# Kernel optimization log

Hardware: AMD Instinct MI355X
Metric: run time of the kernel (lower is better)

Reference implementation:

```python
import jax, jax.numpy as jnp
import numpy as np

B, C, H, W = 2, 256, 64, 64  # C = in_channels; x has 2*C channels
DQ = C // 16


def setup_inputs() -> dict:
    key = jax.random.key(0)
    ks = jax.random.split(key, 10)
    s = 0.05
    return {
        "x": jax.random.normal(ks[0], (B, 2 * C, H, W), dtype=jnp.float32),
        "Wq": jax.random.normal(ks[1], (DQ, C), dtype=jnp.float32) * s,
        "bq": jax.random.normal(ks[2], (DQ,), dtype=jnp.float32) * s,
        "Wk": jax.random.normal(ks[3], (DQ, C), dtype=jnp.float32) * s,
        "bk": jax.random.normal(ks[4], (DQ,), dtype=jnp.float32) * s,
        "Wv": jax.random.normal(ks[5], (C, C), dtype=jnp.float32) * s,
        "bv": jax.random.normal(ks[6], (C,), dtype=jnp.float32) * s,
        "Wpt": jax.random.normal(ks[7], (C, 2 * C), dtype=jnp.float32) * s,
        "bpt": jax.random.normal(ks[8], (C,), dtype=jnp.float32) * s,
        "gamma": jnp.full((1,), 0.5, dtype=jnp.float32),  # original inits to 0; nonzero for a non-trivial output
    }


def _conv1x1(x, Wt, b):
    # 1x1 conv == per-pixel linear map over channels
    return jnp.einsum("bchw,dc->bdhw", x, Wt) + b[None, :, None, None]


def reference(x, Wq, bq, Wk, bk, Wv, bv, Wpt, bpt, gamma):
    n = x.shape[1] // 2
    x1, x2 = x[:, :n], x[:, n:]
    b, c, h, w = x1.shape
    hw = h * w

    def qkv(xi):
        q = _conv1x1(xi, Wq, bq).reshape(b, DQ, hw)   # [B,dq,HW]
        k = _conv1x1(xi, Wk, bk).reshape(b, DQ, hw)   # [B,dq,HW]
        v = _conv1x1(xi, Wv, bv).reshape(b, c, hw)    # [B,C,HW]
        return q, k, v

    q1, k1, v1 = qkv(x1)
    q2, k2, v2 = qkv(x2)

    # attn[b,i,j] = softmax_j( q[:,i] . k[:,j] )  (no scaling, as in original)
    attn1 = jax.nn.softmax(jnp.einsum("bdi,bdj->bij", q1, k1), axis=-1)  # [B,HW,HW]
    attn2 = jax.nn.softmax(jnp.einsum("bdi,bdj->bij", q2, k2), axis=-1)

    def apply_attn(v, attn):
        # out[b,c,i] = sum_j v[b,c,j] * attn[b,i,j]
        return jnp.einsum("bcj,bij->bci", v, attn).reshape(b, c, h, w)

    out11 = apply_attn(v1, attn1)
    out12 = apply_attn(v2, attn1)
    out21 = apply_attn(v1, attn2)
    out22 = apply_attn(v2, attn2)

    o1 = _conv1x1(jnp.concatenate([out11, out12], axis=1), Wpt, bpt)  # [B,C,H,W]
    o2 = _conv1x1(jnp.concatenate([out21, out22], axis=1), Wpt, bpt)

    out = gamma * jnp.concatenate([o1, o2], axis=1) + x
    return out
```

## Files before the change

### kernel.cpp

```cpp
#include <hip/hip_runtime.h>
#include <hip/hip_bf16.h>


#define HW 4096
#define CC 256
#define DQ 16

typedef __hip_bfloat16 bf16;
struct alignas(8) bh4 { bf16 x, y, z, w; };
typedef __bf16 bf16x8 __attribute__((ext_vector_type(8)));
typedef float  f32x4  __attribute__((ext_vector_type(4)));

static __device__ __forceinline__ float b2f(bf16 v) { return __bfloat162float(v); }
static __device__ __forceinline__ float ldf(const void* p, size_t i, bool isb) {
    return isb ? b2f(((const bf16*)p)[i]) : ((const float*)p)[i];
}

static __device__ __forceinline__ void load_lds16(const void* g, void* l) {
    __builtin_amdgcn_global_load_lds(
        (const __attribute__((address_space(1))) unsigned int*)g,
        (__attribute__((address_space(3))) unsigned int*)l, 16, 0, 0);
}

static __device__ __forceinline__ bf16x8 ones8() {
    union { unsigned int u[4]; bf16x8 v; } t;
    t.u[0] = t.u[1] = t.u[2] = t.u[3] = 0x3F803F80u;
    return t.v;
}

__global__ void __launch_bounds__(256)
prep_xt(const void* __restrict__ xsrc,
        const void* __restrict__ Wq_r, const void* __restrict__ bq_r,
        const void* __restrict__ Wk_r, const void* __restrict__ bk_r,
        const void* __restrict__ Wv_r, const void* __restrict__ bv_r,
        const void* __restrict__ Wpt_r, const void* __restrict__ bpt_r,
        const void* __restrict__ gam_r,
        float* __restrict__ bqf, float* __restrict__ bkf, float* __restrict__ gamf,
        bf16* __restrict__ Wqb, bf16* __restrict__ Wkb,
        bf16* __restrict__ McB, float* __restrict__ btot, bf16* __restrict__ Xt,
        const unsigned short* __restrict__ probe) {
    __shared__ float T[64][65];
    int bx = blockIdx.x, tid = threadIdx.x;
    bool isb = probe[0] != 0;
    if (bx < 512) {
        int d = bx >> 1;
        int c = ((bx & 1) << 8) + tid;
        int half = c >> 8, cm = c & 255;
        float acc = 0.f;
        for (int e = 0; e < 256; ++e)
            acc = fmaf(ldf(Wpt_r, (size_t)d * 512 + half * 256 + e, isb),
                       ldf(Wv_r, (size_t)e * 256 + cm, isb), acc);
        McB[d * 512 + c] = __float2bfloat16(acc);
    } else if (bx == 512) {
        int d = tid;
        float acc = ldf(bpt_r, d, isb);
        for (int e = 0; e < 256; ++e)
            acc = fmaf(ldf(Wpt_r, (size_t)d * 512 + e, isb) +
                       ldf(Wpt_r, (size_t)d * 512 + 256 + e, isb),
                       ldf(bv_r, e, isb), acc);
        btot[d] = acc;
    } else if (bx < 545) {
        int id = bx - 513;
        const void* s = id < 16 ? Wq_r : Wk_r;
        bf16* dst = id < 16 ? Wqb : Wkb;
        int i = (id & 15) * 256 + tid;
        dst[i] = __float2bfloat16(ldf(s, i, isb));
    } else if (bx == 545) {
        if (tid < 16) bqf[tid] = ldf(bq_r, tid, isb);
        else if (tid < 32) bkf[tid - 16] = ldf(bk_r, tid - 16, isb);
        else if (tid == 32) gamf[0] = ldf(gam_r, 0, isb);
    } else {
        int id = bx - 546;
        int j0 = (id & 63) * 64, e0 = ((id >> 6) & 7) * 64, b = id >> 9;
        int j_l = tid & 63, er0 = (tid >> 6) * 16;
#pragma unroll
        for (int r = 0; r < 16; ++r) {
            size_t src = ((size_t)(b * 512 + e0 + er0 + r)) * HW + j0 + j_l;
            T[er0 + r][j_l] = ldf(xsrc, src, isb);
        }
        __syncthreads();
        int e_w = tid & 63, jr0 = (tid >> 6) * 16;
#pragma unroll
        for (int r = 0; r < 16; ++r)
            Xt[((size_t)b * HW + j0 + jr0 + r) * 512 + e0 + e_w] =
                __float2bfloat16(T[e_w][jr0 + r]);
    }
}

__global__ void __launch_bounds__(256, 2)
qku(const bf16* __restrict__ Xt,
    const bf16* __restrict__ Wqb, const float* __restrict__ bqf,
    const bf16* __restrict__ Wkb, const float* __restrict__ bkf,
    bf16* __restrict__ Qb, bf16* __restrict__ Kb,
    const bf16* __restrict__ McB, bf16* __restrict__ Ub) {
    __shared__ __align__(16) bf16 sA[64 * 64];
    __shared__ __align__(16) bf16 sB[128 * 64];
    int tid = threadIdx.x;
    int lane = tid & 63, wave = tid >> 6;
    int ln = lane & 15, q = lane >> 4;
    int bx = blockIdx.x;

    if (bx < 256) {
        int bh = bx >> 6;
        int b = bh >> 1, h = bh & 1;
        int j0 = (bx & 63) * 64 + wave * 16;
        bf16x8 aQ[8], aK[8];
#pragma unroll
        for (int kk = 0; kk < 8; ++kk) {
            aQ[kk] = *(const bf16x8*)&Wqb[ln * 256 + kk * 32 + q * 8];
            aK[kk] = *(const bf16x8*)&Wkb[ln * 256 + kk * 32 + q * 8];
        }
        const bf16* Xrow = Xt + ((size_t)b * HW + j0 + ln) * 512 + h * 256;
        f32x4 dQ = {0.f, 0.f, 0.f, 0.f}, dK = {0.f, 0.f, 0.f, 0.f};
#pragma unroll
        for (int kk = 0; kk < 8; ++kk) {
            bf16x8 bxv = *(const bf16x8*)&Xrow[kk * 32 + q * 8];
            dQ = __builtin_amdgcn_mfma_f32_16x16x32_bf16(aQ[kk], bxv, dQ, 0, 0, 0);
            dK = __builtin_amdgcn_mfma_f32_16x16x32_bf16(aK[kk], bxv, dK, 0, 0, 0);
        }
        size_t rowoff = ((size_t)bh * HW + j0 + ln) * 32;
        bh4 oq, ok;
        oq.x = __float2bfloat16(dQ[0] + bqf[q * 4 + 0]);
        oq.y = __float2bfloat16(dQ[1] + bqf[q * 4 + 1]);
        oq.z = __float2bfloat16(dQ[2] + bqf[q * 4 + 2]);
        oq.w = __float2bfloat16(dQ[3] + bqf[q * 4 + 3]);
        ok.x = __float2bfloat16(dK[0] + bkf[q * 4 + 0]);
        ok.y = __float2bfloat16(dK[1] + bkf[q * 4 + 1]);
        ok.z = __float2bfloat16(dK[2] + bkf[q * 4 + 2]);
        ok.w = __float2bfloat16(dK[3] + bkf[q * 4 + 3]);
        bh4 z; z.x = z.y = z.z = z.w = __float2bfloat16(0.f);
        *(bh4*)&Qb[rowoff + q * 4] = oq;
        *(bh4*)&Qb[rowoff + 16 + q * 4] = z;
        *(bh4*)&Kb[rowoff + q * 4] = ok;
        *(bh4*)&Kb[rowoff + 16 + q * 4] = z;
        return;
    }

    int id = bx - 256;
    int wm = (wave >> 1) * 32, wn = (wave & 1) * 64;
    int j0 = (id & 31) * 128, c0 = ((id >> 5) & 3) * 64, b = id >> 7;
    const bf16* Xb = Xt + (size_t)b * HW * 512;
    f32x4 acc[2][4];
#pragma unroll
    for (int mi = 0; mi < 2; ++mi)
#pragma unroll
        for (int ni = 0; ni < 4; ++ni)
#pragma unroll
            for (int r = 0; r < 4; ++r) acc[mi][ni][r] = 0.f;

    for (int e0 = 0; e0 < 512; e0 += 64) {
        __syncthreads();
#pragma unroll
        for (int r = 0; r < 2; ++r) {
            int s = r * 256 + tid;
            int row = s >> 3, jc = s & 7, jg = jc ^ (row & 7);
            load_lds16(McB + (size_t)(c0 + row) * 512 + e0 + jg * 8, sA + s * 8);
        }
#pragma unroll
        for (int r = 0; r < 4; ++r) {
            int s = r * 256 + tid;
            int row = s >> 3, jc = s & 7, jg = jc ^ (row & 7);
            load_lds16(Xb + (size_t)(j0 + row) * 512 + e0 + jg * 8, sB + s * 8);
        }
        __syncthreads();
#pragma unroll
        for (int kh = 0; kh < 2; ++kh) {
            bf16x8 af[2], bfv[4];
#pragma unroll
            for (int mi = 0; mi < 2; ++mi) {
                int row = wm + mi * 16 + ln;
                int jc = (kh * 4 + q) ^ (row & 7);
                af[mi] = *(const bf16x8*)&sA[row * 64 + jc * 8];
            }
#pragma unroll
            for (int ni = 0; ni < 4; ++ni) {
                int row = wn + ni * 16 + ln;
                int jc = (kh * 4 + q) ^ (row & 7);
                bfv[ni] = *(const bf16x8*)&sB[row * 64 + jc * 8];
            }
#pragma unroll
            for (int mi = 0; mi < 2; ++mi)
#pragma unroll
                for (int ni = 0; ni < 4; ++ni)
                    acc[mi][ni] = __builtin_amdgcn_mfma_f32_16x16x32_bf16(
                        af[mi], bfv[ni], acc[mi][ni], 0, 0, 0);
        }
    }
#pragma unroll
    for (int mi = 0; mi < 2; ++mi)
#pragma unroll
        for (int r = 0; r < 4; ++r) {
            int c = c0 + wm + mi * 16 + q * 4 + r;
#pragma unroll
            for (int ni = 0; ni < 4; ++ni) {
                int j = j0 + wn + ni * 16 + ln;
                Ub[((size_t)(b * CC + c)) * HW + j] = __float2bfloat16(acc[mi][ni][r]);
            }
        }
}

__global__ void __launch_bounds__(256, 2)
flash_attn(const bf16* __restrict__ Ub, const bf16* __restrict__ Qb,
           const bf16* __restrict__ Kb, const float* __restrict__ btot,
           const void* __restrict__ xorig, const float* __restrict__ gamf,
           void* __restrict__ outv, const unsigned short* __restrict__ probe) {
    __shared__ __align__(16) bf16 sU[3][128 * 64];
    __shared__ __align__(16) bf16 sK[3][4 * 64 * 8];
    __shared__ __align__(16) bf16 sE[2][64 * 64];
    int tid  = threadIdx.x;
    int lane = tid & 63, wave = tid >> 6;
    int ln = lane & 15, q = lane >> 4;
    int wm = (wave & 1) * 64, wn = (wave >> 1) * 32;
    int i0 = blockIdx.x * 64, c0 = blockIdx.y * 128;
    int bh = blockIdx.z;
    int b = bh >> 1, h = bh & 1;
    const bf16* Ubb = Ub + (size_t)b * CC * HW + (size_t)c0 * HW;
    const bf16* Kbh = Kb + (size_t)bh * HW * 32;
    const bf16x8 ONE = ones8();

    bf16x8 bq = *(const bf16x8*)&Qb[((size_t)bh * HW + i0 + wave * 16 + ln) * 32 + q * 8];

    f32x4 acc[4][2], accS[2];
#pragma unroll
    for (int ni = 0; ni < 2; ++ni) {
#pragma unroll
        for (int r = 0; r < 4; ++r) accS[ni][r] = 0.f;
#pragma unroll
        for (int mi = 0; mi < 4; ++mi)
#pragma unroll
            for (int r = 0; r < 4; ++r) acc[mi][ni][r] = 0.f;
    }

    int i_loc = wave * 16 + ln;
    int wchunk0 = (q >> 1);
    int woff = (q & 1) * 4;

    auto stage_u = [&](int tn, int bufn) {
#pragma unroll
        for (int r = 0; r < 4; ++r) {
            int s = r * 256 + tid;
            int row = s >> 3, jc = s & 7, jg = jc ^ (row & 7);
            load_lds16(Ubb + (size_t)row * HW + tn * 64 + jg * 8, &sU[bufn][s * 8]);
        }
    };
    auto stage_k = [&](int tn, int bufn) {
        load_lds16(Kbh + ((size_t)(tn * 64 + (tid >> 6) * 16 + (tid & 15))) * 32
                       + ((tid >> 4) & 3) * 8,
                   &sK[bufn][tid * 8]);
    };

    stage_u(0, 0);
    stage_k(0, 0);
    stage_k(1, 1);
    asm volatile("s_waitcnt vmcnt(0)" ::: "memory");
    __builtin_amdgcn_sched_barrier(0);
    __builtin_amdgcn_s_barrier();
    __builtin_amdgcn_sched_barrier(0);

    int bu_r = 0, bu_s = 1, bk_r = 0, bk_s = 2;
    for (int t = 0; t < 64; ++t) {
        stage_u((t + 1) & 63, bu_s);
        stage_k((t + 2) & 63, bk_s);

        const bf16* sKc = sK[bk_r];
        bf16* sEc = sE[t & 1];
#pragma unroll
        for (int js = 0; js < 4; ++js) {
            bf16x8 ak = *(const bf16x8*)&sKc[(js * 64 + lane) * 8];
            f32x4 d = {0.f, 0.f, 0.f, 0.f};
            d = __builtin_amdgcn_mfma_f32_16x16x32_bf16(ak, bq, d, 0, 0, 0);
            bh4 o;
            o.x = __float2bfloat16(__expf(d[0]));
            o.y = __float2bfloat16(__expf(d[1]));
            o.z = __float2bfloat16(__expf(d[2]));
            o.w = __float2bfloat16(__expf(d[3]));
            int chunk = (js * 2 + wchunk0) ^ (i_loc & 7);
            *(bh4*)&sEc[i_loc * 64 + chunk * 8 + woff] = o;
        }

        asm volatile("s_waitcnt vmcnt(5) lgkmcnt(0)" ::: "memory");
        __builtin_amdgcn_sched_barrier(0);
        __builtin_amdgcn_s_barrier();
        __builtin_amdgcn_sched_barrier(0);

        const bf16* sUc = sU[bu_r];
        __builtin_amdgcn_s_setprio(1);
#pragma unroll
        for (int kh = 0; kh < 2; ++kh) {
            bf16x8 af[4], bfv[2];
#pragma unroll
            for (int mi = 0; mi < 4; ++mi) {
                int row = wm + mi * 16 + ln;
                int jc = (kh * 4 + q) ^ (row & 7);
                af[mi] = *(const bf16x8*)&sUc[row * 64 + jc * 8];
            }
#pragma unroll
            for (int ni = 0; ni < 2; ++ni) {
                int row = wn + ni * 16 + ln;
                int jc = (kh * 4 + q) ^ (row & 7);
                bfv[ni] = *(const bf16x8*)&sEc[row * 64 + jc * 8];
            }
#pragma unroll
            for (int ni = 0; ni < 2; ++ni) {
                accS[ni] = __builtin_amdgcn_mfma_f32_16x16x32_bf16(
                    ONE, bfv[ni], accS[ni], 0, 0, 0);
#pragma unroll
                for (int mi = 0; mi < 4; ++mi)
                    acc[mi][ni] = __builtin_amdgcn_mfma_f32_16x16x32_bf16(
                        af[mi], bfv[ni], acc[mi][ni], 0, 0, 0);
            }
        }
        __builtin_amdgcn_s_setprio(0);

        bu_r = bu_r == 2 ? 0 : bu_r + 1;
        bu_s = bu_s == 2 ? 0 : bu_s + 1;
        bk_r = bk_r == 2 ? 0 : bk_r + 1;
        bk_s = bk_s == 2 ? 0 : bk_s + 1;
    }

    bool isb = probe[0] != 0;
    float g = gamf[0];
    float lv[2];
#pragma unroll
    for (int ni = 0; ni < 2; ++ni)
        lv[ni] = 1.f / accS[ni][0];
#pragma unroll
    for (int mi = 0; mi < 4; ++mi)
#pragma unroll
        for (int r = 0; r < 4; ++r) {
            int c = c0 + wm + mi * 16 + q * 4 + r;
            float bt = btot[c];
            size_t rowbase = ((size_t)(b * 512 + h * 256 + c)) * HW + i0 + wn;
#pragma unroll
            for (int ni = 0; ni < 2; ++ni) {
                size_t idx = rowbase + ni * 16 + ln;
                float xres = isb ? b2f(((const bf16*)xorig)[idx]) : ((const float*)xorig)[idx];
                float o = fmaf(g, fmaf(acc[mi][ni][r], lv[ni], bt), xres);
                if (isb) ((bf16*)outv)[idx] = __float2bfloat16(o);
                else     ((float*)outv)[idx] = o;
            }
        }
}

extern "C" void kernel_launch(void* const* d_in, const int* in_sizes, int n_in,
                              void* d_out, int out_size, void* d_ws, size_t ws_size,
                              hipStream_t stream) {
    const unsigned short* probe = (const unsigned short*)d_in[9];

    char* ws = (char*)d_ws;
    size_t off = 0;
    auto alloc = [&](size_t bytes) { size_t r = off; off = (off + bytes + 255) & ~(size_t)255; return r; };
    float* bqf  = (float*)(ws + alloc(16 * 4));
    float* bkf  = (float*)(ws + alloc(16 * 4));
    float* gamf = (float*)(ws + alloc(4));
    bf16*  Xt   = (bf16*)(ws + alloc((size_t)2 * HW * 512 * 2));
    bf16*  McB  = (bf16*)(ws + alloc(256 * 512 * 2));
    float* btot = (float*)(ws + alloc(256 * 4));
    bf16*  Wqb  = (bf16*)(ws + alloc(DQ * 256 * 2));
    bf16*  Wkb  = (bf16*)(ws + alloc(DQ * 256 * 2));
    bf16*  Qb   = (bf16*)(ws + alloc((size_t)4 * HW * 32 * 2));
    bf16*  Kb   = (bf16*)(ws + alloc((size_t)4 * HW * 32 * 2));
    bf16*  Ub   = (bf16*)(ws + alloc((size_t)2 * CC * HW * 2));

    prep_xt<<<dim3(1570), 256, 0, stream>>>(
        d_in[0], d_in[1], d_in[2], d_in[3], d_in[4], d_in[5], d_in[6],
        d_in[7], d_in[8], d_in[9],
        bqf, bkf, gamf, Wqb, Wkb, McB, btot, Xt, probe);

    qku<<<dim3(512), 256, 0, stream>>>(Xt, Wqb, bqf, Wkb, bkf, Qb, Kb, McB, Ub);

    flash_attn<<<dim3(64, 2, 4), 256, 0, stream>>>(Ub, Qb, Kb, btot, d_in[0], gamf, d_out, probe);
}
```

Baseline: 249.0 us.

## Shrink flash_attn channel tile to 64 and compute softmax row sums in scalar code

The flash_attn block now covers 64 output channels instead of 128, so the grid doubles and each wave owns one 16-row channel slice. Launch bounds rise so four blocks can share a CU. Softmax row sums are now added up in registers from the rounded exponentials and reduced through shared memory, replacing the extra MFMA against a ones vector. Staging moves from triple to double buffering with a full vmcnt(0) barrier every iteration. The trade is more occupancy and less LDS per block against recomputing QK^T and exp twice as often and losing some load/compute overlap.

Result: slower. 256.5 us (+3.0%).

```diff
diff --git a/kernel.cpp b/kernel.cpp
--- a/kernel.cpp
+++ b/kernel.cpp
@@ -20,12 +20,6 @@
     __builtin_amdgcn_global_load_lds(
         (const __attribute__((address_space(1))) unsigned int*)g,
         (__attribute__((address_space(3))) unsigned int*)l, 16, 0, 0);
-}
-
-static __device__ __forceinline__ bf16x8 ones8() {
-    union { unsigned int u[4]; bf16x8 v; } t;
-    t.u[0] = t.u[1] = t.u[2] = t.u[3] = 0x3F803F80u;
-    return t.v;
 }
 
 __global__ void __launch_bounds__(256)
@@ -199,45 +193,41 @@
         }
 }
 
-__global__ void __launch_bounds__(256, 2)
+__global__ void __launch_bounds__(256, 4)
 flash_attn(const bf16* __restrict__ Ub, const bf16* __restrict__ Qb,
            const bf16* __restrict__ Kb, const float* __restrict__ btot,
            const void* __restrict__ xorig, const float* __restrict__ gamf,
            void* __restrict__ outv, const unsigned short* __restrict__ probe) {
-    __shared__ __align__(16) bf16 sU[3][128 * 64];
-    __shared__ __align__(16) bf16 sK[3][4 * 64 * 8];
-    __shared__ __align__(16) bf16 sE[2][64 * 64];
+    __shared__ __align__(16) bf16 sU[2][64 * 64];
+    __shared__ __align__(16) bf16 sK[2][4 * 64 * 8];
+    __shared__ __align__(16) bf16 sE[64 * 64];
+    __shared__ float sL[64];
     int tid  = threadIdx.x;
     int lane = tid & 63, wave = tid >> 6;
     int ln = lane & 15, q = lane >> 4;
-    int wm = (wave & 1) * 64, wn = (wave >> 1) * 32;
-    int i0 = blockIdx.x * 64, c0 = blockIdx.y * 128;
+    int i0 = blockIdx.x * 64, c0 = blockIdx.y * 64;
     int bh = blockIdx.z;
     int b = bh >> 1, h = bh & 1;
     const bf16* Ubb = Ub + (size_t)b * CC * HW + (size_t)c0 * HW;
     const bf16* Kbh = Kb + (size_t)bh * HW * 32;
-    const bf16x8 ONE = ones8();
 
     bf16x8 bq = *(const bf16x8*)&Qb[((size_t)bh * HW + i0 + wave * 16 + ln) * 32 + q * 8];
 
-    f32x4 acc[4][2], accS[2];
-#pragma unroll
-    for (int ni = 0; ni < 2; ++ni) {
-#pragma unroll
-        for (int r = 0; r < 4; ++r) accS[ni][r] = 0.f;
-#pragma unroll
-        for (int mi = 0; mi < 4; ++mi)
-#pragma unroll
-            for (int r = 0; r < 4; ++r) acc[mi][ni][r] = 0.f;
-    }
+    f32x4 acc[4];
+#pragma unroll
+    for (int ni = 0; ni < 4; ++ni)
+#pragma unroll
+        for (int r = 0; r < 4; ++r) acc[ni][r] = 0.f;
+    float lsum = 0.f;
 
     int i_loc = wave * 16 + ln;
     int wchunk0 = (q >> 1);
     int woff = (q & 1) * 4;
+    int urow = wave * 16 + ln;
 
     auto stage_u = [&](int tn, int bufn) {
 #pragma unroll
-        for (int r = 0; r < 4; ++r) {
+        for (int r = 0; r < 2; ++r) {
             int s = r * 256 + tid;
             int row = s >> 3, jc = s & 7, jg = jc ^ (row & 7);
             load_lds16(Ubb + (size_t)row * HW + tn * 64 + jg * 8, &sU[bufn][s * 8]);
@@ -251,19 +241,16 @@
 
     stage_u(0, 0);
     stage_k(0, 0);
-    stage_k(1, 1);
     asm volatile("s_waitcnt vmcnt(0)" ::: "memory");
     __builtin_amdgcn_sched_barrier(0);
     __builtin_amdgcn_s_barrier();
     __builtin_amdgcn_sched_barrier(0);
 
-    int bu_r = 0, bu_s = 1, bk_r = 0, bk_s = 2;
     for (int t = 0; t < 64; ++t) {
-        stage_u((t + 1) & 63, bu_s);
-        stage_k((t + 2) & 63, bk_s);
-
-        const bf16* sKc = sK[bk_r];
-        bf16* sEc = sE[t & 1];
+        stage_u((t + 1) & 63, (t + 1) & 1);
+        stage_k((t + 1) & 63, (t + 1) & 1);
+
+        const bf16* sKc = sK[t & 1];
 #pragma unroll
         for (int js = 0; js < 4; ++js) {
             bf16x8 ak = *(const bf16x8*)&sKc[(js * 64 + lane) * 8];
@@ -274,72 +261,67 @@
             o.y = __float2bfloat16(__expf(d[1]));
             o.z = __float2bfloat16(__expf(d[2]));
             o.w = __float2bfloat16(__expf(d[3]));
+            lsum += b2f(o.x) + b2f(o.y) + b2f(o.z) + b2f(o.w);
             int chunk = (js * 2 + wchunk0) ^ (i_loc & 7);
-            *(bh4*)&sEc[i_loc * 64 + chunk * 8 + woff] = o;
-        }
-
-        asm volatile("s_waitcnt vmcnt(5) lgkmcnt(0)" ::: "memory");
+            *(bh4*)&sE[i_loc * 64 + chunk * 8 + woff] = o;
+        }
+
+        asm volatile("s_waitcnt lgkmcnt(0)" ::: "memory");
         __builtin_amdgcn_sched_barrier(0);
         __builtin_amdgcn_s_barrier();
         __builtin_amdgcn_sched_barrier(0);
 
-        const bf16* sUc = sU[bu_r];
+        const bf16* sUc = sU[t & 1];
         __builtin_amdgcn_s_setprio(1);
 #pragma unroll
         for (int kh = 0; kh < 2; ++kh) {
-            bf16x8 af[4], bfv[2];
-#pragma unroll
-            for (int mi = 0; mi < 4; ++mi) {
-                int row = wm + mi * 16 + ln;
+            int jca = (kh * 4 + q) ^ (urow & 7);
+            bf16x8 af = *(const bf16x8*)&sUc[urow * 64 + jca * 8];
+            bf16x8 bfv[4];
+#pragma unroll
+            for (int ni = 0; ni < 4; ++ni) {
+                int row = ni * 16 + ln;
                 int jc = (kh * 4 + q) ^ (row & 7);
-                af[mi] = *(const bf16x8*)&sUc[row * 64 + jc * 8];
+                bfv[ni] = *(const bf16x8*)&sE[row * 64 + jc * 8];
             }
 #pragma unroll
-            for (int ni = 0; ni < 2; ++ni) {
-                int row = wn + ni * 16 + ln;
-                int jc = (kh * 4 + q) ^ (row & 7);
-                bfv[ni] = *(const bf16x8*)&sEc[row * 64 + jc * 8];
-            }
-#pragma unroll
-            for (int ni = 0; ni < 2; ++ni) {
-                accS[ni] = __builtin_amdgcn_mfma_f32_16x16x32_bf16(
-                    ONE, bfv[ni], accS[ni], 0, 0, 0);
-#pragma unroll
-                for (int mi = 0; mi < 4; ++mi)
-                    acc[mi][ni] = __builtin_amdgcn_mfma_f32_16x16x32_bf16(
-                        af[mi], bfv[ni], acc[mi][ni], 0, 0, 0);
-            }
+            for (int ni = 0; ni < 4; ++ni)
+                acc[ni] = __builtin_amdgcn_mfma_f32_16x16x32_bf16(
+                    af, bfv[ni], acc[ni], 0, 0, 0);
         }
         __builtin_amdgcn_s_setprio(0);
 
-        bu_r = bu_r == 2 ? 0 : bu_r + 1;
-        bu_s = bu_s == 2 ? 0 : bu_s + 1;
-        bk_r = bk_r == 2 ? 0 : bk_r + 1;
-        bk_s = bk_s == 2 ? 0 : bk_s + 1;
-    }
+        asm volatile("s_waitcnt vmcnt(0) lgkmcnt(0)" ::: "memory");
+        __builtin_amdgcn_sched_barrier(0);
+        __builtin_amdgcn_s_barrier();
+        __builtin_amdgcn_sched_barrier(0);
+    }
+
+    lsum += __shfl_xor(lsum, 16);
+    lsum += __shfl_xor(lsum, 32);
+    if (lane < 16) sL[wave * 16 + lane] = lsum;
+    __syncthreads();
 
     bool isb = probe[0] != 0;
     float g = gamf[0];
-    float lv[2];
-#pragma unroll
-    for (int ni = 0; ni < 2; ++ni)
-        lv[ni] = 1.f / accS[ni][0];
-#pragma unroll
-    for (int mi = 0; mi < 4; ++mi)
-#pragma unroll
-        for (int r = 0; r < 4; ++r) {
-            int c = c0 + wm + mi * 16 + q * 4 + r;
-            float bt = btot[c];
-            size_t rowbase = ((size_t)(b * 512 + h * 256 + c)) * HW + i0 + wn;
-#pragma unroll
-            for (int ni = 0; ni < 2; ++ni) {
-                size_t idx = rowbase + ni * 16 + ln;
-                float xres = isb ? b2f(((const bf16*)xorig)[idx]) : ((const float*)xorig)[idx];
-                float o = fmaf(g, fmaf(acc[mi][ni][r], lv[ni], bt), xres);
-                if (isb) ((bf16*)outv)[idx] = __float2bfloat16(o);
-                else     ((float*)outv)[idx] = o;
-            }
-        }
+    float lv[4];
+#pragma unroll
+    for (int ni = 0; ni < 4; ++ni)
+        lv[ni] = 1.f / sL[ni * 16 + ln];
+#pragma unroll
+    for (int r = 0; r < 4; ++r) {
+        int c = c0 + wave * 16 + q * 4 + r;
+        float bt = btot[c];
+        size_t rowbase = ((size_t)(b * 512 + h * 256 + c)) * HW + i0;
+#pragma unroll
+        for (int ni = 0; ni < 4; ++ni) {
+            size_t idx = rowbase + ni * 16 + ln;
+            float xres = isb ? b2f(((const bf16*)xorig)[idx]) : ((const float*)xorig)[idx];
+            float o = fmaf(g, fmaf(acc[ni][r], lv[ni], bt), xres);
+            if (isb) ((bf16*)outv)[idx] = __float2bfloat16(o);
+            else     ((float*)outv)[idx] = o;
+        }
+    }
 }
 
 extern "C" void kernel_launch(void* const* d_in, const int* in_sizes, int n_in,
@@ -369,5 +351,5 @@
 
     qku<<<dim3(512), 256, 0, stream>>>(Xt, Wqb, bqf, Wkb, bkf, Qb, Kb, McB, Ub);
 
-    flash_attn<<<dim3(64, 2, 4), 256, 0, stream>>>(Ub, Qb, Kb, btot, d_in[0], gamf, d_out, probe);
-}
+    flash_attn<<<dim3(64, 4, 4), 256, 0, stream>>>(Ub, Qb, Kb, btot, d_in[0], gamf, d_out, probe);
+}
```

## Widen flash-attn key tile to 128, load K via registers, sum softmax in VALU

Applied to the files above, without the earlier changes.

The flash attention loop now processes 128 keys per step with a double-buffered U tile instead of 64 keys with triple buffering. K fragments are loaded straight into registers and ping-ponged between two register sets rather than staged through LDS. The row-sum of exp is accumulated with scalar adds and cross-lane shuffles instead of an extra MFMA against a ones vector. This halves barrier and iteration overhead and removes the extra MFMA work, but it uses more LDS and registers per block, which may lower occupancy, and it adds a second barrier per step.

Result: faster. 243.0 us (-2.4%).

```diff
diff --git a/kernel.cpp b/kernel.cpp
--- a/kernel.cpp
+++ b/kernel.cpp
@@ -20,12 +20,6 @@
     __builtin_amdgcn_global_load_lds(
         (const __attribute__((address_space(1))) unsigned int*)g,
         (__attribute__((address_space(3))) unsigned int*)l, 16, 0, 0);
-}
-
-static __device__ __forceinline__ bf16x8 ones8() {
-    union { unsigned int u[4]; bf16x8 v; } t;
-    t.u[0] = t.u[1] = t.u[2] = t.u[3] = 0x3F803F80u;
-    return t.v;
 }
 
 __global__ void __launch_bounds__(256)
@@ -204,9 +198,8 @@
            const bf16* __restrict__ Kb, const float* __restrict__ btot,
            const void* __restrict__ xorig, const float* __restrict__ gamf,
            void* __restrict__ outv, const unsigned short* __restrict__ probe) {
-    __shared__ __align__(16) bf16 sU[3][128 * 64];
-    __shared__ __align__(16) bf16 sK[3][4 * 64 * 8];
-    __shared__ __align__(16) bf16 sE[2][64 * 64];
+    __shared__ __align__(16) bf16 sU[2][128 * 128];
+    __shared__ __align__(16) bf16 sE[64 * 128];
     int tid  = threadIdx.x;
     int lane = tid & 63, wave = tid >> 6;
     int ln = lane & 15, q = lane >> 4;
@@ -216,20 +209,17 @@
     int b = bh >> 1, h = bh & 1;
     const bf16* Ubb = Ub + (size_t)b * CC * HW + (size_t)c0 * HW;
     const bf16* Kbh = Kb + (size_t)bh * HW * 32;
-    const bf16x8 ONE = ones8();
 
     bf16x8 bq = *(const bf16x8*)&Qb[((size_t)bh * HW + i0 + wave * 16 + ln) * 32 + q * 8];
 
-    f32x4 acc[4][2], accS[2];
-#pragma unroll
-    for (int ni = 0; ni < 2; ++ni) {
-#pragma unroll
-        for (int r = 0; r < 4; ++r) accS[ni][r] = 0.f;
-#pragma unroll
-        for (int mi = 0; mi < 4; ++mi)
+    f32x4 acc[4][2];
+#pragma unroll
+    for (int mi = 0; mi < 4; ++mi)
+#pragma unroll
+        for (int ni = 0; ni < 2; ++ni)
 #pragma unroll
             for (int r = 0; r < 4; ++r) acc[mi][ni][r] = 0.f;
-    }
+    float lsum = 0.f;
 
     int i_loc = wave * 16 + ln;
     int wchunk0 = (q >> 1);
@@ -237,93 +227,99 @@
 
     auto stage_u = [&](int tn, int bufn) {
 #pragma unroll
-        for (int r = 0; r < 4; ++r) {
+        for (int r = 0; r < 8; ++r) {
             int s = r * 256 + tid;
-            int row = s >> 3, jc = s & 7, jg = jc ^ (row & 7);
-            load_lds16(Ubb + (size_t)row * HW + tn * 64 + jg * 8, &sU[bufn][s * 8]);
+            int row = s >> 4, jc = s & 15, jg = jc ^ (row & 7);
+            load_lds16(Ubb + (size_t)row * HW + tn * 128 + jg * 8, &sU[bufn][s * 8]);
         }
     };
-    auto stage_k = [&](int tn, int bufn) {
-        load_lds16(Kbh + ((size_t)(tn * 64 + (tid >> 6) * 16 + (tid & 15))) * 32
-                       + ((tid >> 4) & 3) * 8,
-                   &sK[bufn][tid * 8]);
+    auto load_k = [&](int tn, bf16x8 (&kf)[8]) {
+#pragma unroll
+        for (int js = 0; js < 8; ++js)
+            kf[js] = *(const bf16x8*)&Kbh[(size_t)(tn * 128 + js * 16 + ln) * 32 + q * 8];
     };
 
-    stage_u(0, 0);
-    stage_k(0, 0);
-    stage_k(1, 1);
-    asm volatile("s_waitcnt vmcnt(0)" ::: "memory");
-    __builtin_amdgcn_sched_barrier(0);
-    __builtin_amdgcn_s_barrier();
-    __builtin_amdgcn_sched_barrier(0);
-
-    int bu_r = 0, bu_s = 1, bk_r = 0, bk_s = 2;
-    for (int t = 0; t < 64; ++t) {
-        stage_u((t + 1) & 63, bu_s);
-        stage_k((t + 2) & 63, bk_s);
-
-        const bf16* sKc = sK[bk_r];
-        bf16* sEc = sE[t & 1];
-#pragma unroll
-        for (int js = 0; js < 4; ++js) {
-            bf16x8 ak = *(const bf16x8*)&sKc[(js * 64 + lane) * 8];
+    auto iter = [&](int t, bf16x8 (&kf_cur)[8], bf16x8 (&kf_nxt)[8]) {
+        stage_u((t + 1) & 31, (t + 1) & 1);
+
+#pragma unroll
+        for (int js = 0; js < 8; ++js) {
             f32x4 d = {0.f, 0.f, 0.f, 0.f};
-            d = __builtin_amdgcn_mfma_f32_16x16x32_bf16(ak, bq, d, 0, 0, 0);
+            d = __builtin_amdgcn_mfma_f32_16x16x32_bf16(kf_cur[js], bq, d, 0, 0, 0);
             bh4 o;
             o.x = __float2bfloat16(__expf(d[0]));
             o.y = __float2bfloat16(__expf(d[1]));
             o.z = __float2bfloat16(__expf(d[2]));
             o.w = __float2bfloat16(__expf(d[3]));
+            lsum += b2f(o.x) + b2f(o.y) + b2f(o.z) + b2f(o.w);
             int chunk = (js * 2 + wchunk0) ^ (i_loc & 7);
-            *(bh4*)&sEc[i_loc * 64 + chunk * 8 + woff] = o;
-        }
-
-        asm volatile("s_waitcnt vmcnt(5) lgkmcnt(0)" ::: "memory");
+            *(bh4*)&sE[i_loc * 128 + chunk * 8 + woff] = o;
+        }
+
+        load_k((t + 1) & 31, kf_nxt);
+
+        asm volatile("s_waitcnt lgkmcnt(0)" ::: "memory");
         __builtin_amdgcn_sched_barrier(0);
         __builtin_amdgcn_s_barrier();
         __builtin_amdgcn_sched_barrier(0);
 
-        const bf16* sUc = sU[bu_r];
+        const bf16* sUc = sU[t & 1];
         __builtin_amdgcn_s_setprio(1);
 #pragma unroll
-        for (int kh = 0; kh < 2; ++kh) {
+        for (int kh = 0; kh < 4; ++kh) {
             bf16x8 af[4], bfv[2];
 #pragma unroll
             for (int mi = 0; mi < 4; ++mi) {
                 int row = wm + mi * 16 + ln;
                 int jc = (kh * 4 + q) ^ (row & 7);
-                af[mi] = *(const bf16x8*)&sUc[row * 64 + jc * 8];
+                af[mi] = *(const bf16x8*)&sUc[row * 128 + jc * 8];
             }
 #pragma unroll
             for (int ni = 0; ni < 2; ++ni) {
                 int row = wn + ni * 16 + ln;
                 int jc = (kh * 4 + q) ^ (row & 7);
-                bfv[ni] = *(const bf16x8*)&sEc[row * 64 + jc * 8];
-            }
-#pragma unroll
-            for (int ni = 0; ni < 2; ++ni) {
-                accS[ni] = __builtin_amdgcn_mfma_f32_16x16x32_bf16(
-                    ONE, bfv[ni], accS[ni], 0, 0, 0);
-#pragma unroll
-                for (int mi = 0; mi < 4; ++mi)
+                bfv[ni] = *(const bf16x8*)&sE[row * 128 + jc * 8];
+            }
+#pragma unroll
+            for (int mi = 0; mi < 4; ++mi)
+#pragma unroll
+                for (int ni = 0; ni < 2; ++ni)
                     acc[mi][ni] = __builtin_amdgcn_mfma_f32_16x16x32_bf16(
                         af[mi], bfv[ni], acc[mi][ni], 0, 0, 0);
-            }
         }
         __builtin_amdgcn_s_setprio(0);
 
-        bu_r = bu_r == 2 ? 0 : bu_r + 1;
-        bu_s = bu_s == 2 ? 0 : bu_s + 1;
-        bk_r = bk_r == 2 ? 0 : bk_r + 1;
-        bk_s = bk_s == 2 ? 0 : bk_s + 1;
+        asm volatile("s_waitcnt vmcnt(8) lgkmcnt(0)" ::: "memory");
+        __builtin_amdgcn_sched_barrier(0);
+        __builtin_amdgcn_s_barrier();
+        __builtin_amdgcn_sched_barrier(0);
+    };
+
+    bf16x8 kfA[8], kfB[8];
+    load_k(0, kfA);
+    stage_u(0, 0);
+    asm volatile("s_waitcnt vmcnt(0)" ::: "memory");
+    __builtin_amdgcn_sched_barrier(0);
+    __builtin_amdgcn_s_barrier();
+    __builtin_amdgcn_sched_barrier(0);
+
+    for (int tt = 0; tt < 32; tt += 2) {
+        iter(tt, kfA, kfB);
+        iter(tt + 1, kfB, kfA);
     }
+
+    lsum += __shfl_xor(lsum, 16);
+    lsum += __shfl_xor(lsum, 32);
+    float* sLp = (float*)sE;
+    if (lane < 16) sLp[wave * 16 + lane] = lsum;
+    __syncthreads();
 
     bool isb = probe[0] != 0;
     float g = gamf[0];
     float lv[2];
 #pragma unroll
     for (int ni = 0; ni < 2; ++ni)
-        lv[ni] = 1.f / accS[ni][0];
+        lv[ni] = 1.f / sLp[wn + ni * 16 + ln];
 #pragma unroll
     for (int mi = 0; mi < 4; ++mi)
 #pragma unroll
```

## Switch flash attention to double buffering and remap blocks to a 1D grid

Applied to the files above, without the earlier changes.

Cuts the LDS buffers for U and K from triple to double, uses a single E buffer, and adds a second barrier at the end of each iteration so loads can only run one tile ahead. The grid is flattened to 1D so that consecutive blocks cover the 8 (c0, batch-head) panels of the same query tile. The lower LDS use could allow more resident blocks per CU, and the new ordering may improve L2 reuse of the K and Q data. In exchange, each iteration now ends with a full vmcnt(0) drain and an extra barrier, which reduces overlap between memory loads and MFMA work.

Measured after the change: 245.8 us. No clear change (-1.3%).

```diff
diff --git a/kernel.cpp b/kernel.cpp
--- a/kernel.cpp
+++ b/kernel.cpp
@@ -204,16 +204,21 @@
            const bf16* __restrict__ Kb, const float* __restrict__ btot,
            const void* __restrict__ xorig, const float* __restrict__ gamf,
            void* __restrict__ outv, const unsigned short* __restrict__ probe) {
-    __shared__ __align__(16) bf16 sU[3][128 * 64];
-    __shared__ __align__(16) bf16 sK[3][4 * 64 * 8];
-    __shared__ __align__(16) bf16 sE[2][64 * 64];
+    __shared__ __align__(16) bf16 sU[2][128 * 64];
+    __shared__ __align__(16) bf16 sK[2][4 * 64 * 8];
+    __shared__ __align__(16) bf16 sE[64 * 64];
     int tid  = threadIdx.x;
     int lane = tid & 63, wave = tid >> 6;
     int ln = lane & 15, q = lane >> 4;
     int wm = (wave & 1) * 64, wn = (wave >> 1) * 32;
-    int i0 = blockIdx.x * 64, c0 = blockIdx.y * 128;
-    int bh = blockIdx.z;
+
+    int bid = blockIdx.x;
+    int panel = bid & 7;
+    int i0 = (bid >> 3) * 64;
+    int c0 = (panel & 1) * 128;
+    int bh = panel >> 1;
     int b = bh >> 1, h = bh & 1;
+
     const bf16* Ubb = Ub + (size_t)b * CC * HW + (size_t)c0 * HW;
     const bf16* Kbh = Kb + (size_t)bh * HW * 32;
     const bf16x8 ONE = ones8();
@@ -251,19 +256,16 @@
 
     stage_u(0, 0);
     stage_k(0, 0);
-    stage_k(1, 1);
     asm volatile("s_waitcnt vmcnt(0)" ::: "memory");
     __builtin_amdgcn_sched_barrier(0);
     __builtin_amdgcn_s_barrier();
     __builtin_amdgcn_sched_barrier(0);
 
-    int bu_r = 0, bu_s = 1, bk_r = 0, bk_s = 2;
     for (int t = 0; t < 64; ++t) {
-        stage_u((t + 1) & 63, bu_s);
-        stage_k((t + 2) & 63, bk_s);
-
-        const bf16* sKc = sK[bk_r];
-        bf16* sEc = sE[t & 1];
+        stage_u((t + 1) & 63, (t + 1) & 1);
+        stage_k((t + 1) & 63, (t + 1) & 1);
+
+        const bf16* sKc = sK[t & 1];
 #pragma unroll
         for (int js = 0; js < 4; ++js) {
             bf16x8 ak = *(const bf16x8*)&sKc[(js * 64 + lane) * 8];
@@ -275,15 +277,15 @@
             o.z = __float2bfloat16(__expf(d[2]));
             o.w = __float2bfloat16(__expf(d[3]));
             int chunk = (js * 2 + wchunk0) ^ (i_loc & 7);
-            *(bh4*)&sEc[i_loc * 64 + chunk * 8 + woff] = o;
-        }
-
-        asm volatile("s_waitcnt vmcnt(5) lgkmcnt(0)" ::: "memory");
+            *(bh4*)&sE[i_loc * 64 + chunk * 8 + woff] = o;
+        }
+
+        asm volatile("s_waitcnt lgkmcnt(0)" ::: "memory");
         __builtin_amdgcn_sched_barrier(0);
         __builtin_amdgcn_s_barrier();
         __builtin_amdgcn_sched_barrier(0);
 
-        const bf16* sUc = sU[bu_r];
+        const bf16* sUc = sU[t & 1];
         __builtin_amdgcn_s_setprio(1);
 #pragma unroll
         for (int kh = 0; kh < 2; ++kh) {
@@ -298,7 +300,7 @@
             for (int ni = 0; ni < 2; ++ni) {
                 int row = wn + ni * 16 + ln;
                 int jc = (kh * 4 + q) ^ (row & 7);
-                bfv[ni] = *(const bf16x8*)&sEc[row * 64 + jc * 8];
+                bfv[ni] = *(const bf16x8*)&sE[row * 64 + jc * 8];
             }
 #pragma unroll
             for (int ni = 0; ni < 2; ++ni) {
@@ -312,10 +314,10 @@
         }
         __builtin_amdgcn_s_setprio(0);
 
-        bu_r = bu_r == 2 ? 0 : bu_r + 1;
-        bu_s = bu_s == 2 ? 0 : bu_s + 1;
-        bk_r = bk_r == 2 ? 0 : bk_r + 1;
-        bk_s = bk_s == 2 ? 0 : bk_s + 1;
+        asm volatile("s_waitcnt vmcnt(0) lgkmcnt(0)" ::: "memory");
+        __builtin_amdgcn_sched_barrier(0);
+        __builtin_amdgcn_s_barrier();
+        __builtin_amdgcn_sched_barrier(0);
     }
 
     bool isb = probe[0] != 0;
@@ -369,5 +371,5 @@
 
     qku<<<dim3(512), 256, 0, stream>>>(Xt, Wqb, bqf, Wkb, bkf, Qb, Kb, McB, Ub);
 
-    flash_attn<<<dim3(64, 2, 4), 256, 0, stream>>>(Ub, Qb, Kb, btot, d_in[0], gamf, d_out, probe);
-}
+    flash_attn<<<dim3(512), 256, 0, stream>>>(Ub, Qb, Kb, btot, d_in[0], gamf, d_out, probe);
+}
```
